# Performance work log

Hardware: AMD Instinct MI355X
Metric: run time of the kernel (lower is better)

## Reference

```python
import jax, jax.numpy as jnp
import numpy as np

# dims
B, Nt, Ln, Lv = 16, 64, 256, 4      # batch, trees/batch, nodes/tree, value tokens/node
D = 256                              # embedding_dim
VOCAB, NTYPE = 32000, 64
M, Ls = 128, 4                       # story memory slots, tokens per slot
HOPS = 3                             # max_hops
COMP_STEP = 4                        # max tree depth = max(kb_n_layers)
LEVELS = [0, 1, 16, 64, 160, Ln]     # node index ranges per depth 0..4


def setup_inputs() -> dict:
    rng = np.random.default_rng(0)
    key = jax.random.key(0)
    ks = jax.random.split(key, 12)

    # --- tree structure: depth per node, father index in previous level ---
    depth = np.zeros(Ln, np.int64)
    father = np.zeros((B, Nt, Ln), np.int64)
    for lvl in range(1, 5):
        lo, hi = LEVELS[lvl], LEVELS[lvl + 1]
        depth[lo:hi] = lvl
        father[..., lo:hi] = rng.integers(LEVELS[lvl - 1], LEVELS[lvl], (B, Nt, hi - lo))
    father[..., 0] = Ln  # root's father = pad slot (torch -1 wraps to last index)
    kb_fathers = np.concatenate([father, np.full((B, Nt, 1), Ln, np.int64)], -1)  # [B,Nt,Ln+1]
    nl = np.broadcast_to(depth, (B, Nt, Ln))
    kb_n_layers = np.concatenate([nl, np.full((B, Nt, 1), -1, np.int64)], -1)     # [B,Nt,Ln+1]

    kb_values = rng.integers(1, VOCAB, (B, Nt, Ln, Lv))
    kb_types = rng.integers(1, NTYPE, (B, Nt, Ln))
    story = rng.integers(1, VOCAB, (B, M, Ls))
    decoder_input = rng.integers(1, VOCAB, (B,))

    s = 1.0 / np.sqrt(D)
    C = 0.1 * jax.random.normal(ks[0], (HOPS + 1, VOCAB, D), jnp.float32)
    C = C.at[:, 0].set(0.0)  # padding_idx = 0
    T_emb = 0.1 * jax.random.normal(ks[1], (NTYPE, D), jnp.float32)
    T_emb = T_emb.at[0].set(0.0)
    return {
        'decoder_input': jnp.asarray(decoder_input),
        'story': jnp.asarray(story),
        'hidden': 0.1 * jax.random.normal(ks[2], (1, B, D), jnp.float32),
        'kb_values': jnp.asarray(kb_values),
        'kb_types': jnp.asarray(kb_types),
        'kb_fathers': jnp.asarray(kb_fathers),
        'kb_n_layers': jnp.asarray(kb_n_layers),
        'C': C,
        'T_emb': T_emb,
        'Wq': s * jax.random.normal(ks[3], (D, D), jnp.float32),
        'Wk': s * jax.random.normal(ks[4], (D, D), jnp.float32),
        'Wv': s * jax.random.normal(ks[5], (D, D), jnp.float32),
        'W1_w': s * jax.random.normal(ks[6], (VOCAB, 2 * D), jnp.float32),
        'W1_b': jnp.zeros((VOCAB,), jnp.float32),
        'W_ih': s * jax.random.normal(ks[7], (3 * D, D), jnp.float32),
        'W_hh': s * jax.random.normal(ks[8], (3 * D, D), jnp.float32),
        'b_ih': jnp.zeros((3 * D,), jnp.float32),
        'b_hh': jnp.zeros((3 * D,), jnp.float32),
    }


def _forward(decoder_input, story, hidden, kb_values, kb_types, kb_fathers, kb_n_layers,
             C, T_emb, Wq, Wk, Wv, W1_w, W1_b, W_ih, W_hh, b_ih, b_hh):
    C0 = C[0]
    # ensemble: node embed = type_embed * sum(value token embeds)   [B,Nt,Ln,D]
    node = T_emb[kb_types] * C0[kb_values].sum(-2)
    node = jnp.concatenate([node, jnp.zeros((B, Nt, 1, D), node.dtype)], axis=2)  # pad slot
    nl = COMP_STEP - 1 - kb_n_layers  # adjusted layer counter
    base = jnp.arange(B * Nt).reshape(B, Nt, 1) * (Ln + 1)
    seg = (base + kb_fathers).reshape(-1)  # flat father ids for scatter-add

    def body(i, carry):
        node, nl = carry
        nxt = jax.ops.segment_sum(node.reshape(-1, D), seg,
                                  num_segments=B * Nt * (Ln + 1)).reshape(B, Nt, Ln + 1, D)
        node = node + nxt * (nl == 0)[..., None].astype(node.dtype)
        return (node, nl - 1)

    node, _ = jax.lax.fori_loop(0, COMP_STEP, body, (node, nl))
    roots = node[:, :, 0]                                   # [B,Nt,D]
    bias = jnp.where(roots.sum(-1) == 0, -1e9, 0.0)         # attention_bias [B,Nt]

    # compute_global_ranking: QKV attention over tree roots
    h = hidden[-1]                                          # [B,D]
    w = jax.nn.softmax(jnp.einsum('bnd,bd->bn', roots @ Wk.T, h @ Wq.T) + bias, axis=1)
    feat = jnp.einsum('bn,bnd->bd', w, roots @ Wv.T)        # kb_attn_features

    # single GRU step (PyTorch gate order r,z,n)
    x = C0[decoder_input]
    gi = x @ W_ih.T + b_ih
    gh = h @ W_hh.T + b_hh
    ir, iz, inn = jnp.split(gi, 3, -1)
    hr, hz, hn = jnp.split(gh, 3, -1)
    r = jax.nn.sigmoid(ir + hr)
    z = jax.nn.sigmoid(iz + hz)
    n = jnp.tanh(inn + r * hn)
    h_new = (1.0 - z) * n + z * h
    u = h_new + feat                                        # cur_state

    # ptrMemDecoder (Mem2Seq-style hops over story memory)
    p_vocab = None
    logits = None
    for hop in range(HOPS):
        m_A = C[hop][story].sum(2)                          # [B,M,D]
        logits = jnp.einsum('bmd,bd->bm', m_A, u)
        prob = jax.nn.softmax(logits, axis=1)
        m_C = C[hop + 1][story].sum(2)
        o = jnp.einsum('bm,bmd->bd', prob, m_C)
        if hop == 0:
            p_vocab = jnp.concatenate([u, o], -1) @ W1_w.T + W1_b
        u = u + o
    p_ptr = logits
    return p_ptr, p_vocab, h_new


def reference(decoder_input, story, hidden, kb_values, kb_types, kb_fathers, kb_n_layers,
              C, T_emb, Wq, Wk, Wv, W1_w, W1_b, W_ih, W_hh, b_ih, b_hh):
    return _forward(decoder_input, story, hidden, kb_values, kb_types, kb_fathers, kb_n_layers,
                    C, T_emb, Wq, Wk, Wv, W1_w, W1_b, W_ih, W_hh, b_ih, b_hh)
```

## Files before the change

kernel.cpp:

```cpp
#include <hip/hip_runtime.h>
#include <hip/hip_bf16.h>
#include <math.h>

#define B_ 16
#define NT 64
#define LN 256
#define LV 4
#define D_ 256
#define VOCAB_ 32000
#define M_ 128
#define LS 4
#define ECAP 352

typedef unsigned short ushort_t;
typedef unsigned int uint_t;

__device__ __forceinline__ ushort_t f2bf(float f) {
  uint_t u = __float_as_uint(f);
  uint_t r = u + 0x7FFFu + ((u >> 16) & 1u);
  return (ushort_t)(r >> 16);
}
__device__ __forceinline__ float bflo(uint_t u) {
  return __uint_as_float(u << 16);
}
__device__ __forceinline__ float bfhi(uint_t u) {
  return __uint_as_float(u & 0xFFFF0000u);
}

#define NB_S (3 * B_ * M_)
#define NB_CONV 2048
#define NB_TR 192
#define NB_TQK 256
#define NB_WVT 64
#define NB_BKT (B_ * NT)
__global__ __launch_bounds__(256) void k_prep(
    const int* __restrict__ story, const float* __restrict__ C,
    const float* __restrict__ W_ih, const float* __restrict__ W_hh,
    const float* __restrict__ Wq, const float* __restrict__ Wk,
    const float* __restrict__ Wv, const int* __restrict__ kb_values,
    const int* __restrict__ kb_types, float* __restrict__ S,
    ushort_t* __restrict__ C0h, float* __restrict__ W_ihT,
    float* __restrict__ W_hhT, float* __restrict__ TQK,
    float* __restrict__ WvT, int* __restrict__ entries,
    int* __restrict__ counts) {
  __shared__ __align__(16) char praw[6400];
  float* smem = (float*)praw;
  int blk = blockIdx.x, tid = threadIdx.x;
  if (blk < NB_S) {
    int h = blk / (B_ * M_);
    int bm = blk % (B_ * M_);
    const int* st = story + (size_t)bm * LS;
    const float* Ch = C + (size_t)h * VOCAB_ * D_;
    float s = Ch[(size_t)st[0] * D_ + tid] + Ch[(size_t)st[1] * D_ + tid] +
              Ch[(size_t)st[2] * D_ + tid] + Ch[(size_t)st[3] * D_ + tid];
    S[(size_t)blk * D_ + tid] = s;
  } else if (blk < NB_S + NB_CONV) {
    int n4 = VOCAB_ * D_ / 4;
    for (int i = (blk - NB_S) * 256 + tid; i < n4; i += NB_CONV * 256) {
      float4 f = ((const float4*)C)[i];
      uint2 packed;
      packed.x = (uint_t)f2bf(f.x) | ((uint_t)f2bf(f.y) << 16);
      packed.y = (uint_t)f2bf(f.z) | ((uint_t)f2bf(f.w) << 16);
      ((uint2*)C0h)[i] = packed;
    }
  } else if (blk < NB_S + NB_CONV + 2 * NB_TR) {
    int t = blk - (NB_S + NB_CONV);
    const float* W = W_ih;
    float* WT = W_ihT;
    if (t >= NB_TR) { t -= NB_TR; W = W_hh; WT = W_hhT; }
    const int R = 768;
    int tr = t % (R / 32), tc = t / (R / 32);
    int tx = tid & 31, ty = tid >> 5;
#pragma unroll
    for (int k = 0; k < 4; ++k)
      smem[(ty + 8 * k) * 33 + tx] =
          W[(size_t)(tr * 32 + ty + 8 * k) * D_ + tc * 32 + tx];
    __syncthreads();
#pragma unroll
    for (int k = 0; k < 4; ++k)
      WT[(size_t)(tc * 32 + ty + 8 * k) * R + tr * 32 + tx] =
          smem[tx * 33 + ty + 8 * k];
  } else if (blk < NB_S + NB_CONV + 2 * NB_TR + NB_TQK) {
    int j = blk - (NB_S + NB_CONV + 2 * NB_TR);
    smem[tid] = Wq[(size_t)tid * D_ + j];
    __syncthreads();
    float acc = 0.f;
#pragma unroll 8
    for (int k = 0; k < D_; ++k) acc += smem[k] * Wk[(size_t)k * D_ + tid];
    TQK[(size_t)j * D_ + tid] = acc;
  } else if (blk < NB_S + NB_CONV + 2 * NB_TR + NB_TQK + NB_WVT) {
    int t = blk - (NB_S + NB_CONV + 2 * NB_TR + NB_TQK);
    int tr = t & 7, tc = t >> 3;
    int tx = tid & 31, ty = tid >> 5;
#pragma unroll
    for (int k = 0; k < 4; ++k)
      smem[(ty + 8 * k) * 33 + tx] =
          Wv[(size_t)(tr * 32 + ty + 8 * k) * D_ + tc * 32 + tx];
    __syncthreads();
#pragma unroll
    for (int k = 0; k < 4; ++k)
      WvT[(size_t)(tc * 32 + ty + 8 * k) * D_ + tr * 32 + tx] =
          smem[tx * 33 + ty + 8 * k];
  } else {
    int bn = blk - (NB_S + NB_CONV + 2 * NB_TR + NB_TQK + NB_WVT);
    int* sval = (int*)praw;
    int* stype = sval + 1024;
    int* sbin = stype + 256;
    int* srng = sbin + 256;
    const int* vp = kb_values + (size_t)bn * LN * LV;
    for (int i = tid; i < LN * LV; i += 256) sval[i] = vp[i];
    stype[tid] = kb_types[(size_t)bn * LN + tid];
    sbin[tid] = 0;
    __syncthreads();
    int ty = stype[tid];
    int vv[4];
#pragma unroll
    for (int j = 0; j < 4; ++j) {
      vv[j] = sval[tid * 4 + j];
      atomicAdd(&sbin[((vv[j] >> 13) << 6) | ty], 1);
    }
    __syncthreads();
    if (tid < 64) {
      int run = 0;
#pragma unroll
      for (int c = 0; c < 4; ++c) {
        int x = sbin[c * 64 + tid];
        int orig = x;
        for (int o = 1; o < 64; o <<= 1) {
          int y = __shfl_up(x, o);
          if ((int)tid >= o) x += y;
        }
        sbin[c * 64 + tid] = x - orig + run;
        run += __shfl(x, 63);
      }
    }
    __syncthreads();
    if (tid < 4) {
      srng[tid] = sbin[tid << 6];
      int e = (tid == 3) ? (LN * LV) : sbin[(tid + 1) << 6];
      counts[bn * 4 + tid] = min(e - sbin[tid << 6], ECAP);
    }
    __syncthreads();
#pragma unroll
    for (int j = 0; j < 4; ++j) {
      int v = vv[j];
      int r = v >> 13;
      int pos = atomicAdd(&sbin[(r << 6) | ty], 1) - srng[r];
      if (pos < ECAP)
        entries[(size_t)(bn * 4 + r) * ECAP + pos] = v | (ty << 16);
    }
  }
}

#define NBG 512
__global__ __launch_bounds__(512) void k_rootsg(
    const int* __restrict__ counts, const int* __restrict__ entries,
    const ushort_t* __restrict__ C0h, const float* __restrict__ T_emb,
    const int* __restrict__ dec, const float* __restrict__ C0,
    const float* __restrict__ hidden, const float* __restrict__ W_ihT,
    const float* __restrict__ W_hhT, const float* __restrict__ TQK,
    const float* __restrict__ b_ih, const float* __restrict__ b_hh,
    float* __restrict__ part, float* __restrict__ gi, float* __restrict__ gh,
    float* __restrict__ tvec) {
  __shared__ __align__(16) char smem_raw[64512];
  int blk = blockIdx.x, tid = threadIdx.x;
  if (blk < NBG) {
    const float4* Tg = (const float4*)(T_emb + D_);
    float4* t4s = (float4*)smem_raw;
    for (int i = tid; i < 63 * 64; i += 512) t4s[i] = Tg[i];
    __syncthreads();
    int wid = tid >> 6, lane = tid & 63;
    int slot = blk & 7;
    int r = slot >> 1, sub = slot & 1;
    int bn = (((blk >> 3) << 1) | sub) * 8 + wid;
    int bucket = bn * 4 + r;
    int cnt = counts[bucket];
    const int* ge = entries + (size_t)bucket * ECAP;
    const int4* ge4 = (const int4*)ge;
    float a0 = 0.f, a1 = 0.f, a2 = 0.f, a3 = 0.f;
    int k = 0;
#pragma unroll 2
    for (; k + 4 <= cnt; k += 4) {
      int4 e4 = ge4[k >> 2];
      int ex = __builtin_amdgcn_readfirstlane(e4.x);
      int ey = __builtin_amdgcn_readfirstlane(e4.y);
      int ez = __builtin_amdgcn_readfirstlane(e4.z);
      int ew = __builtin_amdgcn_readfirstlane(e4.w);
      uint2 u0 = ((const uint2*)(C0h + ((size_t)(ex & 0xFFFF) << 8)))[lane];
      uint2 u1 = ((const uint2*)(C0h + ((size_t)(ey & 0xFFFF) << 8)))[lane];
      uint2 u2 = ((const uint2*)(C0h + ((size_t)(ez & 0xFFFF) << 8)))[lane];
      uint2 u3 = ((const uint2*)(C0h + ((size_t)(ew & 0xFFFF) << 8)))[lane];
      float4 t0 = t4s[((ex >> 16) - 1) * 64 + lane];
      float4 t1 = t4s[((ey >> 16) - 1) * 64 + lane];
      float4 t2 = t4s[((ez >> 16) - 1) * 64 + lane];
      float4 t3 = t4s[((ew >> 16) - 1) * 64 + lane];
      a0 += t0.x * bflo(u0.x) + t1.x * bflo(u1.x) + t2.x * bflo(u2.x) +
            t3.x * bflo(u3.x);
      a1 += t0.y * bfhi(u0.x) + t1.y * bfhi(u1.x) + t2.y * bfhi(u2.x) +
            t3.y * bfhi(u3.x);
      a2 += t0.z * bflo(u0.y) + t1.z * bflo(u1.y) + t2.z * bflo(u2.y) +
            t3.z * bflo(u3.y);
      a3 += t0.w * bfhi(u0.y) + t1.w * bfhi(u1.y) + t2.w * bfhi(u2.y) +
            t3.w * bfhi(u3.y);
    }
    for (; k < cnt; ++k) {
      int e = __builtin_amdgcn_readfirstlane(ge[k]);
      uint2 u = ((const uint2*)(C0h + ((size_t)(e & 0xFFFF) << 8)))[lane];
      float4 t = t4s[((e >> 16) - 1) * 64 + lane];
      a0 += t.x * bflo(u.x);
      a1 += t.y * bfhi(u.x);
      a2 += t.z * bflo(u.y);
      a3 += t.w * bfhi(u.y);
    }
    float4 res;
    res.x = a0; res.y = a1; res.z = a2; res.w = a3;
    ((float4*)(part + (size_t)bucket * D_))[lane] = res;
  } else {
    int g = blk - NBG;
    float* xs = (float*)smem_raw;
    float acc[B_];
    int i = (g < 3 ? g : g - 3) * 256 + tid;
    if (g < 3) {
      float bias = (tid < 256) ? b_ih[i] : 0.f;
#pragma unroll
      for (int b = 0; b < B_; ++b) acc[b] = bias;
      for (int c = 0; c < 4; ++c) {
        __syncthreads();
        for (int idx = tid; idx < B_ * 64; idx += 512) {
          int b = idx >> 6, jj = idx & 63;
          xs[idx] = C0[(size_t)dec[b] * D_ + c * 64 + jj];
        }
        __syncthreads();
        if (tid < 256) {
#pragma unroll 4
          for (int jj = 0; jj < 64; ++jj) {
            float w = W_ihT[(size_t)(c * 64 + jj) * 768 + i];
#pragma unroll
            for (int b = 0; b < B_; ++b) acc[b] += xs[b * 64 + jj] * w;
          }
        }
      }
      if (tid < 256) {
#pragma unroll
        for (int b = 0; b < B_; ++b) gi[(size_t)b * 768 + i] = acc[b];
      }
    } else if (g < 6) {
      float bias = (tid < 256) ? b_hh[i] : 0.f;
#pragma unroll
      for (int b = 0; b < B_; ++b) acc[b] = bias;
      for (int c = 0; c < 4; ++c) {
        __syncthreads();
        for (int idx = tid; idx < B_ * 64; idx += 512) {
          int b = idx >> 6, jj = idx & 63;
          xs[idx] = hidden[b * D_ + c * 64 + jj];
        }
        __syncthreads();
        if (tid < 256) {
#pragma unroll 4
          for (int jj = 0; jj < 64; ++jj) {
            float w = W_hhT[(size_t)(c * 64 + jj) * 768 + i];
#pragma unroll
            for (int b = 0; b < B_; ++b) acc[b] += xs[b * 64 + jj] * w;
          }
        }
      }
      if (tid < 256) {
#pragma unroll
        for (int b = 0; b < B_; ++b) gh[(size_t)b * 768 + i] = acc[b];
      }
    } else {
#pragma unroll
      for (int b = 0; b < B_; ++b) acc[b] = 0.f;
      for (int c = 0; c < 4; ++c) {
        __syncthreads();
        for (int idx = tid; idx < B_ * 64; idx += 512) {
          int b = idx >> 6, jj = idx & 63;
          xs[idx] = hidden[b * D_ + c * 64 + jj];
        }
        __syncthreads();
        if (tid < 256) {
#pragma unroll 4
          for (int jj = 0; jj < 64; ++jj) {
            float w = TQK[(size_t)(c * 64 + jj) * D_ + tid];
#pragma unroll
            for (int b = 0; b < B_; ++b) acc[b] += xs[b * 64 + jj] * w;
          }
        }
      }
      if (tid < 256) {
#pragma unroll
        for (int b = 0; b < B_; ++b) tvec[b * D_ + tid] = acc[b];
      }
    }
  }
}

__global__ __launch_bounds__(256) void k_mid(
    const float* __restrict__ part, const float* __restrict__ tvec,
    const float* __restrict__ S, float* __restrict__ scores,
    float* __restrict__ ST, float* __restrict__ rsum) {
  int blk = blockIdx.x, tid = threadIdx.x;
  if (blk < 1024) {
    int b = blk >> 6;
    const float* p = part + (size_t)blk * 4 * D_;
    float rv = p[tid] + p[D_ + tid] + p[2 * D_ + tid] + p[3 * D_ + tid];
    rsum[(size_t)blk * D_ + tid] = rv;
    float sc = rv * tvec[b * D_ + tid];
    float sm = rv;
    __shared__ float red[8];
    int lane = tid & 63, wave = tid >> 6;
    for (int o = 32; o > 0; o >>= 1) {
      sc += __shfl_xor(sc, o);
      sm += __shfl_xor(sm, o);
    }
    if (lane == 0) { red[wave] = sc; red[4 + wave] = sm; }
    __syncthreads();
    if (tid == 0) {
      float SC = red[0] + red[1] + red[2] + red[3];
      float SM = red[4] + red[5] + red[6] + red[7];
      scores[blk] = (SM == 0.0f) ? SC - 1000000000.0f : SC;
    }
  } else {
    int t = blk - 1024;
    int hb = t >> 5;
    int tile = t & 31;
    int tm = tile & 3, td = tile >> 2;
    int tx = tid & 31, ty = tid >> 5;
    __shared__ float sm2[32 * 33];
    const float* Sp = S + (size_t)hb * M_ * D_;
    float* STp = ST + (size_t)hb * D_ * M_;
#pragma unroll
    for (int k = 0; k < 4; ++k)
      sm2[(ty + 8 * k) * 33 + tx] =
          Sp[(size_t)(tm * 32 + ty + 8 * k) * D_ + td * 32 + tx];
    __syncthreads();
#pragma unroll
    for (int k = 0; k < 4; ++k)
      STp[(size_t)(td * 32 + ty + 8 * k) * M_ + tm * 32 + tx] =
          sm2[tx * 33 + ty + 8 * k];
  }
}

__global__ __launch_bounds__(256) void k_chain(
    const float* __restrict__ scores, const float* __restrict__ rsum,
    const float* __restrict__ WvT, const float* __restrict__ gi,
    const float* __restrict__ gh, const float* __restrict__ hidden,
    const float* __restrict__ S, const float* __restrict__ ST,
    float* __restrict__ h_new_out, float* __restrict__ cat,
    float* __restrict__ p_ptr) {
  int b = blockIdx.x, tid = threadIdx.x;
  __shared__ float wsh[NT], rs[D_], us[D_], lo[M_], loB[M_], pr[M_];
  if (tid < NT) {
    float s = scores[b * NT + tid];
    float m = s;
    for (int o = 32; o > 0; o >>= 1) m = fmaxf(m, __shfl_xor(m, o));
    float e = expf(s - m);
    float sum = e;
    for (int o = 32; o > 0; o >>= 1) sum += __shfl_xor(sum, o);
    wsh[tid] = e / sum;
  }
  __syncthreads();
  float rb = 0.f;
#pragma unroll 16
  for (int n = 0; n < NT; ++n)
    rb += wsh[n] * rsum[(size_t)(b * NT + n) * D_ + tid];
  rs[tid] = rb;
  __syncthreads();
  float feat = 0.f;
#pragma unroll 16
  for (int j = 0; j < D_; ++j) feat += rs[j] * WvT[(size_t)j * D_ + tid];
  {
    float i_r = gi[(size_t)b * 768 + tid];
    float i_z = gi[(size_t)b * 768 + 256 + tid];
    float i_n = gi[(size_t)b * 768 + 512 + tid];
    float h_r = gh[(size_t)b * 768 + tid];
    float h_z = gh[(size_t)b * 768 + 256 + tid];
    float h_n = gh[(size_t)b * 768 + 512 + tid];
    float h = hidden[b * D_ + tid];
    float r = 1.f / (1.f + expf(-(i_r + h_r)));
    float z = 1.f / (1.f + expf(-(i_z + h_z)));
    float nn = tanhf(i_n + r * h_n);
    float hn = (1.f - z) * nn + z * h;
    h_new_out[b * D_ + tid] = hn;
    float u0 = hn + feat;
    us[tid] = u0;
    cat[b * 512 + tid] = u0;
  }
  __syncthreads();
  for (int h = 0; h < 3; ++h) {
    {
      int m = tid & 127;
      int half = tid >> 7;
      const float* STp = ST + (((size_t)h * B_ + b) * D_ + half * 128) * M_;
      float l = 0.f;
#pragma unroll 16
      for (int d = 0; d < 128; ++d)
        l += us[half * 128 + d] * STp[(size_t)d * M_ + m];
      if (half == 0) lo[m] = l; else loB[m] = l;
    }
    __syncthreads();
    if (h == 2) {
      if (tid < M_) p_ptr[b * M_ + tid] = lo[tid] + loB[tid];
      break;
    }
    if (tid < 64) {
      float l0 = lo[tid] + loB[tid], l1 = lo[tid + 64] + loB[tid + 64];
      float a = fmaxf(l0, l1);
      for (int o = 32; o > 0; o >>= 1) a = fmaxf(a, __shfl_xor(a, o));
      float e0 = expf(l0 - a), e1 = expf(l1 - a);
      float s = e0 + e1;
      for (int o = 32; o > 0; o >>= 1) s += __shfl_xor(s, o);
      pr[tid] = e0 / s;
      pr[tid + 64] = e1 / s;
    }
    __syncthreads();
    {
      const float* Sn = S + (((size_t)(h + 1) * B_ + b) * M_) * D_;
      float o = 0.f;
#pragma unroll 16
      for (int m = 0; m < M_; ++m) o += pr[m] * Sn[(size_t)m * D_ + tid];
      if (h == 0) cat[b * 512 + D_ + tid] = o;
      us[tid] += o;
    }
    __syncthreads();
  }
}

__global__ __launch_bounds__(256) void k_pvocab(
    const float* __restrict__ cat, const float* __restrict__ W1_w,
    const float* __restrict__ W1_b, float* __restrict__ out) {
  int blk = blockIdx.x, tid = threadIdx.x;
  int row = tid & 63, q = tid >> 6;
  int v = blk * 64 + row;
  __shared__ float cs[B_ * 512];
  __shared__ float ps[3][64][B_];
  for (int i = tid; i < B_ * 512; i += 256) cs[i] = cat[i];
  __syncthreads();
  const float4* wrow = (const float4*)(W1_w + (size_t)v * 512 + q * 128);
  float acc[B_];
#pragma unroll
  for (int b = 0; b < B_; ++b) acc[b] = 0.f;
#pragma unroll 4
  for (int k4 = 0; k4 < 32; ++k4) {
    float4 w = wrow[k4];
#pragma unroll
    for (int b = 0; b < B_; ++b) {
      const float* c = &cs[b * 512 + q * 128 + k4 * 4];
      acc[b] += w.x * c[0] + w.y * c[1] + w.z * c[2] + w.w * c[3];
    }
  }
  if (q > 0) {
#pragma unroll
    for (int b = 0; b < B_; ++b) ps[q - 1][row][b] = acc[b];
  }
  __syncthreads();
  if (q == 0) {
    float bb = W1_b[v];
#pragma unroll
    for (int b = 0; b < B_; ++b)
      out[(size_t)b * VOCAB_ + v] =
          acc[b] + ps[0][row][b] + ps[1][row][b] + ps[2][row][b] + bb;
  }
}

extern "C" void kernel_launch(void* const* d_in, const int* in_sizes, int n_in,
                              void* d_out, int out_size, void* d_ws,
                              size_t ws_size, hipStream_t stream) {
  const int* decoder_input = (const int*)d_in[0];
  const int* story = (const int*)d_in[1];
  const float* hidden = (const float*)d_in[2];
  const int* kb_values = (const int*)d_in[3];
  const int* kb_types = (const int*)d_in[4];
  const float* C = (const float*)d_in[7];
  const float* T_emb = (const float*)d_in[8];
  const float* Wq = (const float*)d_in[9];
  const float* Wk = (const float*)d_in[10];
  const float* Wv = (const float*)d_in[11];
  const float* W1_w = (const float*)d_in[12];
  const float* W1_b = (const float*)d_in[13];
  const float* W_ih = (const float*)d_in[14];
  const float* W_hh = (const float*)d_in[15];
  const float* b_ih = (const float*)d_in[16];
  const float* b_hh = (const float*)d_in[17];

  float* out = (float*)d_out;
  float* p_ptr = out;
  float* p_vocab = out + B_ * M_;
  float* h_new = out + B_ * M_ + B_ * VOCAB_;

  float* ws = (float*)d_ws;
  float* S = ws;
  float* part = S + 3 * B_ * M_ * D_;
  float* rsum = part + B_ * NT * 4 * D_;
  float* cat = rsum + B_ * NT * D_;
  float* scores = cat + B_ * 512;
  float* gi = scores + B_ * NT;
  float* gh = gi + B_ * 768;
  float* tvec = gh + B_ * 768;
  int* counts = (int*)(tvec + B_ * D_);
  ushort_t* C0h = (ushort_t*)(counts + 4096);
  float* wtmp = (float*)(C0h + (size_t)VOCAB_ * D_);
  float* W_ihT = wtmp;
  float* W_hhT = W_ihT + 768 * D_;
  float* TQK = W_hhT + 768 * D_;
  int* entries = (int*)(TQK + D_ * D_);
  float* ST = wtmp;
  float* WvT = wtmp + (458752 + 1441792);

  hipLaunchKernelGGL(
      k_prep, dim3(NB_S + NB_CONV + 2 * NB_TR + NB_TQK + NB_WVT + NB_BKT),
      dim3(256), 0, stream, story, C, W_ih, W_hh, Wq, Wk, Wv, kb_values,
      kb_types, S, C0h, W_ihT, W_hhT, TQK, WvT, entries, counts);
  hipLaunchKernelGGL(k_rootsg, dim3(NBG + 7), dim3(512), 0, stream, counts,
                     entries, C0h, T_emb, decoder_input, C, hidden, W_ihT,
                     W_hhT, TQK, b_ih, b_hh, part, gi, gh, tvec);
  hipLaunchKernelGGL(k_mid, dim3(1024 + 1536), dim3(256), 0, stream, part,
                     tvec, S, scores, ST, rsum);
  hipLaunchKernelGGL(k_chain, dim3(B_), dim3(256), 0, stream, scores, rsum,
                     WvT, gi, gh, hidden, S, ST, h_new, cat, p_ptr);
  hipLaunchKernelGGL(k_pvocab, dim3(VOCAB_ / 64), dim3(256), 0, stream, cat,
                     W1_w, W1_b, p_vocab);
}
```

Measured before the change: 389.9 us.

## Assign gather work units per XCD via atomic queue and stage entries in LDS

Each gather block now reads its XCD id from a hardware register and claims a work unit from an atomic per-range counter, preferring the vocab-row range matched to that XCD. The intent is that each XCD's L2 serves mostly one quarter of the bf16 embedding table, which cuts cross-XCD duplication and L2 misses. Entry lists are also copied into LDS before the main loop. This adds an atomic per block, a counter reset in the prep kernel, and a dependence on the block-to-XCD mapping, with a possible load imbalance when ranges run out.

```diff
diff --git a/kernel.cpp b/kernel.cpp
--- a/kernel.cpp
+++ b/kernel.cpp
@@ -42,10 +42,11 @@
     ushort_t* __restrict__ C0h, float* __restrict__ W_ihT,
     float* __restrict__ W_hhT, float* __restrict__ TQK,
     float* __restrict__ WvT, int* __restrict__ entries,
-    int* __restrict__ counts) {
+    int* __restrict__ counts, int* __restrict__ qctr) {
   __shared__ __align__(16) char praw[6400];
   float* smem = (float*)praw;
   int blk = blockIdx.x, tid = threadIdx.x;
+  if (blk == 0 && tid < 8) qctr[tid] = 0;
   if (blk < NB_S) {
     int h = blk / (B_ * M_);
     int bm = blk % (B_ * M_);
@@ -153,6 +154,7 @@
 }
 
 #define NBG 512
+#define UNITS_PER_RANGE 128
 __global__ __launch_bounds__(512) void k_rootsg(
     const int* __restrict__ counts, const int* __restrict__ entries,
     const ushort_t* __restrict__ C0h, const float* __restrict__ T_emb,
@@ -161,27 +163,42 @@
     const float* __restrict__ W_hhT, const float* __restrict__ TQK,
     const float* __restrict__ b_ih, const float* __restrict__ b_hh,
     float* __restrict__ part, float* __restrict__ gi, float* __restrict__ gh,
-    float* __restrict__ tvec) {
-  __shared__ __align__(16) char smem_raw[64512];
+    float* __restrict__ tvec, int* __restrict__ qctr) {
+  __shared__ __align__(16) char smem_raw[64512 + 11264 + 16];
   int blk = blockIdx.x, tid = threadIdx.x;
   if (blk < NBG) {
+    float4* t4s = (float4*)smem_raw;
+    int* ent_all = (int*)(smem_raw + 64512);
+    int* sunit = (int*)(smem_raw + 64512 + 11264);
     const float4* Tg = (const float4*)(T_emb + D_);
-    float4* t4s = (float4*)smem_raw;
     for (int i = tid; i < 63 * 64; i += 512) t4s[i] = Tg[i];
-    __syncthreads();
+    if (tid == 0) {
+      int xcd = __builtin_amdgcn_s_getreg(6164) & 7;
+      int r0 = xcd >> 1;
+      int unit = -1;
+      for (int a = 0; a < 4 && unit < 0; ++a) {
+        int rr = (r0 + a) & 3;
+        int u = atomicAdd(&qctr[rr], 1);
+        if (u < UNITS_PER_RANGE) unit = (u << 2) | rr;
+      }
+      sunit[0] = unit;
+    }
+    __syncthreads();
+    int unit = sunit[0];
+    if (unit < 0) return;
+    int rr = unit & 3, u = unit >> 2;
     int wid = tid >> 6, lane = tid & 63;
-    int slot = blk & 7;
-    int r = slot >> 1, sub = slot & 1;
-    int bn = (((blk >> 3) << 1) | sub) * 8 + wid;
-    int bucket = bn * 4 + r;
+    int bn = u * 8 + wid;
+    int bucket = bn * 4 + rr;
     int cnt = counts[bucket];
     const int* ge = entries + (size_t)bucket * ECAP;
-    const int4* ge4 = (const int4*)ge;
+    int* ent = ent_all + wid * ECAP;
+    for (int i = lane; i < cnt; i += 64) ent[i] = ge[i];
     float a0 = 0.f, a1 = 0.f, a2 = 0.f, a3 = 0.f;
     int k = 0;
 #pragma unroll 2
     for (; k + 4 <= cnt; k += 4) {
-      int4 e4 = ge4[k >> 2];
+      int4 e4 = *(const int4*)(ent + k);
       int ex = __builtin_amdgcn_readfirstlane(e4.x);
       int ey = __builtin_amdgcn_readfirstlane(e4.y);
       int ez = __builtin_amdgcn_readfirstlane(e4.z);
@@ -204,13 +221,14 @@
             t3.w * bfhi(u3.y);
     }
     for (; k < cnt; ++k) {
-      int e = __builtin_amdgcn_readfirstlane(ge[k]);
-      uint2 u = ((const uint2*)(C0h + ((size_t)(e & 0xFFFF) << 8)))[lane];
-      float4 t = t4s[((e >> 16) - 1) * 64 + lane];
-      a0 += t.x * bflo(u.x);
-      a1 += t.y * bfhi(u.x);
-      a2 += t.z * bflo(u.y);
-      a3 += t.w * bfhi(u.y);
+      int e = ent[k];
+      int es = __builtin_amdgcn_readfirstlane(e);
+      uint2 uu = ((const uint2*)(C0h + ((size_t)(es & 0xFFFF) << 8)))[lane];
+      float4 t = t4s[((es >> 16) - 1) * 64 + lane];
+      a0 += t.x * bflo(uu.x);
+      a1 += t.y * bfhi(uu.x);
+      a2 += t.z * bflo(uu.y);
+      a3 += t.w * bfhi(uu.y);
     }
     float4 res;
     res.x = a0; res.y = a1; res.z = a2; res.w = a3;
@@ -498,7 +516,8 @@
   float* gh = gi + B_ * 768;
   float* tvec = gh + B_ * 768;
   int* counts = (int*)(tvec + B_ * D_);
-  ushort_t* C0h = (ushort_t*)(counts + 4096);
+  int* qctr = counts + 4096;
+  ushort_t* C0h = (ushort_t*)(qctr + 8);
   float* wtmp = (float*)(C0h + (size_t)VOCAB_ * D_);
   float* W_ihT = wtmp;
   float* W_hhT = W_ihT + 768 * D_;
@@ -510,10 +529,10 @@
   hipLaunchKernelGGL(
       k_prep, dim3(NB_S + NB_CONV + 2 * NB_TR + NB_TQK + NB_WVT + NB_BKT),
       dim3(256), 0, stream, story, C, W_ih, W_hh, Wq, Wk, Wv, kb_values,
-      kb_types, S, C0h, W_ihT, W_hhT, TQK, WvT, entries, counts);
+      kb_types, S, C0h, W_ihT, W_hhT, TQK, WvT, entries, counts, qctr);
   hipLaunchKernelGGL(k_rootsg, dim3(NBG + 7), dim3(512), 0, stream, counts,
                      entries, C0h, T_emb, decoder_input, C, hidden, W_ihT,
-                     W_hhT, TQK, b_ih, b_hh, part, gi, gh, tvec);
+                     W_hhT, TQK, b_ih, b_hh, part, gi, gh, tvec, qctr);
   hipLaunchKernelGGL(k_mid, dim3(1024 + 1536), dim3(256), 0, stream, part,
                      tvec, S, scores, ST, rsum);
   hipLaunchKernelGGL(k_chain, dim3(B_), dim3(256), 0, stream, scores, rsum,
```

New measurement: 381.2 us. -2.2%, faster.
